# Performance work log

Hardware: AMD Instinct MI355X
Metric: run time of the kernel (lower is better)

The kernel has to match this reference:

```python
import jax, jax.numpy as jnp
import numpy as np

INPUT_SIZE = 128
OUTPUT_SIZE = 128
P_NUM = 16
BATCH = 131072


def setup_inputs() -> dict:
    key = jax.random.key(0)
    k_x, k_c = jax.random.split(key)
    x = jax.random.normal(k_x, (BATCH, INPUT_SIZE), dtype=jnp.float32)
    coef = jax.random.normal(k_c, (OUTPUT_SIZE, INPUT_SIZE, P_NUM), dtype=jnp.float32) * 0.1
    tanh_range = jnp.array(1.0, dtype=jnp.float32)
    return {"x": x, "coef": coef, "tanh_range": tanh_range}


def reference(x, coef, tanh_range):
    # Original: values = tanh(x*t); out[b,o] = sum_i sum_p coef[o,i,p] * values[b,i]
    # Equivalent fused form: (sum_p coef) applied as a single GEMM.
    values = jnp.tanh(x * tanh_range)          # [B, I]
    w = jnp.sum(coef, axis=2)                  # [O, I]
    return jnp.einsum('bi,oi->bo', values, w)  # [B, O]
```

## Files before the change

kernel.cpp:

```cpp
#include <hip/hip_runtime.h>

#define BATCH 131072
#define IN 128
#define OUT 128
#define PNUM 16
#define LDS_PITCH 136

typedef _Float16 f16x8 __attribute__((ext_vector_type(8)));
typedef float f32x4 __attribute__((ext_vector_type(4)));

__global__ __launch_bounds__(256) void prep_w_kernel(const float* __restrict__ coef,
                                                     _Float16* __restrict__ w) {
    int t = blockIdx.x * blockDim.x + threadIdx.x;
    const float4* p = (const float4*)(coef + (size_t)t * PNUM);
    float4 a = p[0], b = p[1], c = p[2], d = p[3];
    float s = (a.x + a.y + a.z + a.w) + (b.x + b.y + b.z + b.w)
            + (c.x + c.y + c.z + c.w) + (d.x + d.y + d.z + d.w);
    w[t] = (_Float16)s;
}

__global__ __launch_bounds__(512, 5) void gemm_tanh_kernel(const float* __restrict__ x,
                                                           const _Float16* __restrict__ w,
                                                           const float* __restrict__ trange,
                                                           float* __restrict__ out) {
    __shared__ _Float16 wlds[OUT * LDS_PITCH];

    const float ts = trange[0] * 2.8853900817779268f;
    const int tid  = threadIdx.x;
    const int lane = tid & 63;
    const int wv   = tid >> 6;
    const int m = lane & 15;
    const int q = lane >> 4;

    const size_t row_base = (size_t)blockIdx.x * 128 + (size_t)wv * 16;
    const float* xrow = x + (row_base + m) * IN;

    f32x4 xv[8];
#pragma unroll
    for (int ks = 0; ks < 4; ++ks) {
        xv[2 * ks]     = *reinterpret_cast<const f32x4*>(xrow + ks * 32 + q * 8);
        xv[2 * ks + 1] = *reinterpret_cast<const f32x4*>(xrow + ks * 32 + q * 8 + 4);
    }

#pragma unroll
    for (int i = 0; i < 4; ++i) {
        int idx = (i * 512 + tid) * 8;
        int r = idx >> 7;
        int c = idx & 127;
        *(f16x8*)&wlds[r * LDS_PITCH + c] = *(const f16x8*)(w + idx);
    }
    __syncthreads();

    f16x8 af[4];
#pragma unroll
    for (int ks = 0; ks < 4; ++ks) {
        f32x4 a = xv[2 * ks], b = xv[2 * ks + 1];
#pragma unroll
        for (int e = 0; e < 4; ++e) {
            float ea = __builtin_amdgcn_exp2f(a[e] * ts);
            float eb = __builtin_amdgcn_exp2f(b[e] * ts);
            af[ks][e]     = (_Float16)__builtin_fmaf(-2.0f, __builtin_amdgcn_rcpf(ea + 1.0f), 1.0f);
            af[ks][e + 4] = (_Float16)__builtin_fmaf(-2.0f, __builtin_amdgcn_rcpf(eb + 1.0f), 1.0f);
        }
    }

    f32x4 acc[8];
#pragma unroll
    for (int nt = 0; nt < 8; ++nt) acc[nt] = (f32x4){0.f, 0.f, 0.f, 0.f};

#pragma unroll
    for (int ks = 0; ks < 4; ++ks) {
        const int kb = ks * 32 + q * 8;
#pragma unroll
        for (int nt = 0; nt < 8; ++nt) {
            f16x8 bf = *(const f16x8*)&wlds[(nt * 16 + m) * LDS_PITCH + kb];
            acc[nt] = __builtin_amdgcn_mfma_f32_16x16x32_f16(bf, af[ks], acc[nt], 0, 0, 0);
        }
    }

    float* orow = out + (row_base + m) * OUT + q * 4;
#pragma unroll
    for (int nt = 0; nt < 8; ++nt) {
        __builtin_nontemporal_store(acc[nt], reinterpret_cast<f32x4*>(orow + nt * 16));
    }
}

extern "C" void kernel_launch(void* const* d_in, const int* in_sizes, int n_in,
                              void* d_out, int out_size, void* d_ws, size_t ws_size,
                              hipStream_t stream) {
    const float* x    = (const float*)d_in[0];
    const float* coef = (const float*)d_in[1];
    const float* tr   = (const float*)d_in[2];
    float* out = (float*)d_out;
    _Float16* w = (_Float16*)d_ws;

    prep_w_kernel<<<(OUT * IN) / 256, 256, 0, stream>>>(coef, w);
    gemm_tanh_kernel<<<BATCH / 128, 512, 0, stream>>>(x, w, tr, out);
}
```

Measured before the change: 122.0 us.

## Make GEMM blocks persistent over several row tiles with double-buffered x prefetch

Blocks now hold 256 threads and each handles 4 successive 64-row tiles. The W tile is staged into LDS once per block and reused across all iterations, and the next tile's x rows are prefetched into registers while the current tile is computed. This amortizes the LDS fill of W and overlaps global loads with tanh and MFMA work. In exchange there are fewer blocks (512), higher register pressure from the double buffer, and less parallelism per CU.

New measurement: 124.7 us. +2.1%, slower.

```diff
diff --git a/kernel.cpp b/kernel.cpp
--- a/kernel.cpp
+++ b/kernel.cpp
@@ -5,6 +5,8 @@
 #define OUT 128
 #define PNUM 16
 #define LDS_PITCH 136
+#define NITER 4
+#define ROWS_PER_BLOCK (64 * NITER)
 
 typedef _Float16 f16x8 __attribute__((ext_vector_type(8)));
 typedef float f32x4 __attribute__((ext_vector_type(4)));
@@ -19,7 +21,7 @@
     w[t] = (_Float16)s;
 }
 
-__global__ __launch_bounds__(512, 5) void gemm_tanh_kernel(const float* __restrict__ x,
+__global__ __launch_bounds__(256, 2) void gemm_tanh_kernel(const float* __restrict__ x,
                                                            const _Float16* __restrict__ w,
                                                            const float* __restrict__ trange,
                                                            float* __restrict__ out) {
@@ -32,56 +34,72 @@
     const int m = lane & 15;
     const int q = lane >> 4;
 
-    const size_t row_base = (size_t)blockIdx.x * 128 + (size_t)wv * 16;
-    const float* xrow = x + (row_base + m) * IN;
-
-    f32x4 xv[8];
 #pragma unroll
-    for (int ks = 0; ks < 4; ++ks) {
-        xv[2 * ks]     = *reinterpret_cast<const f32x4*>(xrow + ks * 32 + q * 8);
-        xv[2 * ks + 1] = *reinterpret_cast<const f32x4*>(xrow + ks * 32 + q * 8 + 4);
-    }
-
-#pragma unroll
-    for (int i = 0; i < 4; ++i) {
-        int idx = (i * 512 + tid) * 8;
+    for (int i = 0; i < 8; ++i) {
+        int idx = (i * 256 + tid) * 8;
         int r = idx >> 7;
         int c = idx & 127;
         *(f16x8*)&wlds[r * LDS_PITCH + c] = *(const f16x8*)(w + idx);
     }
+
+    const size_t base_row = (size_t)blockIdx.x * ROWS_PER_BLOCK + (size_t)wv * 16 + m;
+
+    f32x4 xv[2][8];
+    {
+        const float* xr = x + base_row * IN;
+#pragma unroll
+        for (int ks = 0; ks < 4; ++ks) {
+            xv[0][2 * ks]     = *reinterpret_cast<const f32x4*>(xr + ks * 32 + q * 8);
+            xv[0][2 * ks + 1] = *reinterpret_cast<const f32x4*>(xr + ks * 32 + q * 8 + 4);
+        }
+    }
     __syncthreads();
 
-    f16x8 af[4];
 #pragma unroll
-    for (int ks = 0; ks < 4; ++ks) {
-        f32x4 a = xv[2 * ks], b = xv[2 * ks + 1];
+    for (int it = 0; it < NITER; ++it) {
+        const int cur = it & 1;
+
+        if (it + 1 < NITER) {
+            const float* xr = x + (base_row + (size_t)(it + 1) * 64) * IN;
 #pragma unroll
-        for (int e = 0; e < 4; ++e) {
-            float ea = __builtin_amdgcn_exp2f(a[e] * ts);
-            float eb = __builtin_amdgcn_exp2f(b[e] * ts);
-            af[ks][e]     = (_Float16)__builtin_fmaf(-2.0f, __builtin_amdgcn_rcpf(ea + 1.0f), 1.0f);
-            af[ks][e + 4] = (_Float16)__builtin_fmaf(-2.0f, __builtin_amdgcn_rcpf(eb + 1.0f), 1.0f);
+            for (int ks = 0; ks < 4; ++ks) {
+                xv[cur ^ 1][2 * ks]     = *reinterpret_cast<const f32x4*>(xr + ks * 32 + q * 8);
+                xv[cur ^ 1][2 * ks + 1] = *reinterpret_cast<const f32x4*>(xr + ks * 32 + q * 8 + 4);
+            }
         }
-    }
 
-    f32x4 acc[8];
+        f16x8 af[4];
 #pragma unroll
-    for (int nt = 0; nt < 8; ++nt) acc[nt] = (f32x4){0.f, 0.f, 0.f, 0.f};
+        for (int ks = 0; ks < 4; ++ks) {
+            f32x4 a = xv[cur][2 * ks], b = xv[cur][2 * ks + 1];
+#pragma unroll
+            for (int e = 0; e < 4; ++e) {
+                float ea = __builtin_amdgcn_exp2f(a[e] * ts);
+                float eb = __builtin_amdgcn_exp2f(b[e] * ts);
+                af[ks][e]     = (_Float16)__builtin_fmaf(-2.0f, __builtin_amdgcn_rcpf(ea + 1.0f), 1.0f);
+                af[ks][e + 4] = (_Float16)__builtin_fmaf(-2.0f, __builtin_amdgcn_rcpf(eb + 1.0f), 1.0f);
+            }
+        }
+
+        f32x4 acc[8];
+#pragma unroll
+        for (int nt = 0; nt < 8; ++nt) acc[nt] = (f32x4){0.f, 0.f, 0.f, 0.f};
 
 #pragma unroll
-    for (int ks = 0; ks < 4; ++ks) {
-        const int kb = ks * 32 + q * 8;
+        for (int ks = 0; ks < 4; ++ks) {
+            const int kb = ks * 32 + q * 8;
+#pragma unroll
+            for (int nt = 0; nt < 8; ++nt) {
+                f16x8 bf = *(const f16x8*)&wlds[(nt * 16 + m) * LDS_PITCH + kb];
+                acc[nt] = __builtin_amdgcn_mfma_f32_16x16x32_f16(bf, af[ks], acc[nt], 0, 0, 0);
+            }
+        }
+
+        float* orow = out + (base_row + (size_t)it * 64) * OUT + q * 4;
 #pragma unroll
         for (int nt = 0; nt < 8; ++nt) {
-            f16x8 bf = *(const f16x8*)&wlds[(nt * 16 + m) * LDS_PITCH + kb];
-            acc[nt] = __builtin_amdgcn_mfma_f32_16x16x32_f16(bf, af[ks], acc[nt], 0, 0, 0);
+            __builtin_nontemporal_store(acc[nt], reinterpret_cast<f32x4*>(orow + nt * 16));
         }
-    }
-
-    float* orow = out + (row_base + m) * OUT + q * 4;
-#pragma unroll
-    for (int nt = 0; nt < 8; ++nt) {
-        __builtin_nontemporal_store(acc[nt], reinterpret_cast<f32x4*>(orow + nt * 16));
     }
 }
 
@@ -95,5 +113,5 @@
     _Float16* w = (_Float16*)d_ws;
 
     prep_w_kernel<<<(OUT * IN) / 256, 256, 0, stream>>>(coef, w);
-    gemm_tanh_kernel<<<BATCH / 128, 512, 0, stream>>>(x, w, tr, out);
+    gemm_tanh_kernel<<<BATCH / ROWS_PER_BLOCK, 256, 0, stream>>>(x, w, tr, out);
 }
```

## Coalesce x loads and output stores via per-wave LDS staging, shrink blocks

Applied to the files above, without the earlier changes.

Global loads of x and stores of out now use fully coalesced row-contiguous patterns, with each wave staging its tanh'd fp16 tile and fp32 output tile through a per-wave LDS scratch buffer to transpose into MFMA layout. Blocks shrink from 128 rows and 512 threads to 64 rows and 256 threads, so the weight matrix is copied into LDS twice as often overall. Output stores are no longer nontemporal. The extra LDS round trips and the larger per-block LDS footprint trade against better global memory access efficiency.

Result: faster. 116.1 us (-4.9%).

```diff
diff --git a/kernel.cpp b/kernel.cpp
--- a/kernel.cpp
+++ b/kernel.cpp
@@ -4,9 +4,12 @@
 #define IN 128
 #define OUT 128
 #define PNUM 16
-#define LDS_PITCH 136
+#define WPITCH 136
+#define XPITCH 136
+#define OPITCH 132
 
 typedef _Float16 f16x8 __attribute__((ext_vector_type(8)));
+typedef _Float16 f16x4 __attribute__((ext_vector_type(4)));
 typedef float f32x4 __attribute__((ext_vector_type(4)));
 
 __global__ __launch_bounds__(256) void prep_w_kernel(const float* __restrict__ coef,
@@ -19,49 +22,60 @@
     w[t] = (_Float16)s;
 }
 
-__global__ __launch_bounds__(512, 5) void gemm_tanh_kernel(const float* __restrict__ x,
+__global__ __launch_bounds__(256, 2) void gemm_tanh_kernel(const float* __restrict__ x,
                                                            const _Float16* __restrict__ w,
                                                            const float* __restrict__ trange,
                                                            float* __restrict__ out) {
-    __shared__ _Float16 wlds[OUT * LDS_PITCH];
+    __shared__ _Float16 wlds[OUT * WPITCH];
+    __shared__ __align__(16) unsigned char scratch[4][16 * OPITCH * 4];
 
     const float ts = trange[0] * 2.8853900817779268f;
     const int tid  = threadIdx.x;
     const int lane = tid & 63;
     const int wv   = tid >> 6;
-    const int m = lane & 15;
-    const int q = lane >> 4;
+    const int m    = lane & 15;
+    const int q    = lane >> 4;
+    const int s    = lane & 31;
+    const int half = lane >> 5;
 
-    const size_t row_base = (size_t)blockIdx.x * 128 + (size_t)wv * 16;
-    const float* xrow = x + (row_base + m) * IN;
+#pragma unroll
+    for (int i = 0; i < 8; ++i) {
+        int idx = (i * 256 + tid) * 8;
+        int r = idx >> 7;
+        int c = idx & 127;
+        *(f16x8*)&wlds[r * WPITCH + c] = *(const f16x8*)(w + idx);
+    }
+
+    const int row0 = blockIdx.x * 64 + wv * 16;
 
     f32x4 xv[8];
 #pragma unroll
-    for (int ks = 0; ks < 4; ++ks) {
-        xv[2 * ks]     = *reinterpret_cast<const f32x4*>(xrow + ks * 32 + q * 8);
-        xv[2 * ks + 1] = *reinterpret_cast<const f32x4*>(xrow + ks * 32 + q * 8 + 4);
+    for (int j = 0; j < 8; ++j) {
+        xv[j] = *reinterpret_cast<const f32x4*>(
+            x + (size_t)(row0 + 2 * j + half) * IN + s * 4);
     }
+    __builtin_amdgcn_sched_barrier(0);
+    __syncthreads();
+
+    _Float16* xb = (_Float16*)scratch[wv];
+    float*    ob = (float*)scratch[wv];
 
 #pragma unroll
-    for (int i = 0; i < 4; ++i) {
-        int idx = (i * 512 + tid) * 8;
-        int r = idx >> 7;
-        int c = idx & 127;
-        *(f16x8*)&wlds[r * LDS_PITCH + c] = *(const f16x8*)(w + idx);
+    for (int j = 0; j < 8; ++j) {
+        f32x4 a = xv[j];
+        f16x4 h;
+#pragma unroll
+        for (int e = 0; e < 4; ++e) {
+            float ea = __builtin_amdgcn_exp2f(a[e] * ts);
+            h[e] = (_Float16)__builtin_fmaf(-2.0f, __builtin_amdgcn_rcpf(ea + 1.0f), 1.0f);
+        }
+        *(f16x4*)&xb[(2 * j + half) * XPITCH + s * 4] = h;
     }
-    __syncthreads();
 
     f16x8 af[4];
 #pragma unroll
     for (int ks = 0; ks < 4; ++ks) {
-        f32x4 a = xv[2 * ks], b = xv[2 * ks + 1];
-#pragma unroll
-        for (int e = 0; e < 4; ++e) {
-            float ea = __builtin_amdgcn_exp2f(a[e] * ts);
-            float eb = __builtin_amdgcn_exp2f(b[e] * ts);
-            af[ks][e]     = (_Float16)__builtin_fmaf(-2.0f, __builtin_amdgcn_rcpf(ea + 1.0f), 1.0f);
-            af[ks][e + 4] = (_Float16)__builtin_fmaf(-2.0f, __builtin_amdgcn_rcpf(eb + 1.0f), 1.0f);
-        }
+        af[ks] = *(const f16x8*)&xb[m * XPITCH + ks * 32 + q * 8];
     }
 
     f32x4 acc[8];
@@ -73,15 +87,20 @@
         const int kb = ks * 32 + q * 8;
 #pragma unroll
         for (int nt = 0; nt < 8; ++nt) {
-            f16x8 bf = *(const f16x8*)&wlds[(nt * 16 + m) * LDS_PITCH + kb];
+            f16x8 bf = *(const f16x8*)&wlds[(nt * 16 + m) * WPITCH + kb];
             acc[nt] = __builtin_amdgcn_mfma_f32_16x16x32_f16(bf, af[ks], acc[nt], 0, 0, 0);
         }
     }
 
-    float* orow = out + (row_base + m) * OUT + q * 4;
 #pragma unroll
     for (int nt = 0; nt < 8; ++nt) {
-        __builtin_nontemporal_store(acc[nt], reinterpret_cast<f32x4*>(orow + nt * 16));
+        *(f32x4*)&ob[m * OPITCH + nt * 16 + q * 4] = acc[nt];
+    }
+
+#pragma unroll
+    for (int j = 0; j < 8; ++j) {
+        f32x4 o = *(const f32x4*)&ob[(2 * j + half) * OPITCH + s * 4];
+        *reinterpret_cast<f32x4*>(out + (size_t)(row0 + 2 * j + half) * OUT + s * 4) = o;
     }
 }
 
@@ -95,5 +114,5 @@
     _Float16* w = (_Float16*)d_ws;
 
     prep_w_kernel<<<(OUT * IN) / 256, 256, 0, stream>>>(coef, w);
-    gemm_tanh_kernel<<<BATCH / 128, 512, 0, stream>>>(x, w, tr, out);
+    gemm_tanh_kernel<<<BATCH / 64, 256, 0, stream>>>(x, w, tr, out);
 }
```
